# Optimization experiments

Measured on AMD Instinct MI355X. Metric: run time of the kernel, lower is better.

The kernel has to match this reference:

```python
import jax, jax.numpy as jnp
import numpy as np

B, C, D, E, ES, TOPK = 8, 4096, 1024, 16, 256, 4096

def setup_inputs() -> dict:
    key = jax.random.key(0)
    k1, k2, k3, k4 = jax.random.split(key, 4)
    x = jax.random.normal(k1, (B, C, D), dtype=jnp.float32)
    gate = jax.random.normal(k2, (C, E), dtype=jnp.float32) / np.sqrt(D)
    lin1_weight = jax.random.normal(k3, (D, E, ES), dtype=jnp.float32) / np.sqrt(D)
    lin2_weight = jax.random.normal(k4, (E, ES, D), dtype=jnp.float32) / np.sqrt(ES)
    return {"x": x, "gate": gate, "lin1_weight": lin1_weight, "lin2_weight": lin2_weight, "topk": TOPK}

def reference(x, gate, lin1_weight, lin2_weight, topk):
    b, c, d = x.shape
    e = gate.shape[1]
    n_tokens = b * c
    # faithful to original einsum: sum x over dmodel, elementwise-mult by gate[c, e]
    gate_out = jnp.einsum('bcd,ce->bce', x, gate)            # [b, c, e]
    gate_out = jnp.transpose(gate_out, (2, 0, 1)).reshape(e, n_tokens)
    gate_out = jax.nn.softmax(gate_out, axis=1)              # softmax over tokens per expert
    topk_values, topk_indices = jax.lax.top_k(gate_out, topk)  # [e, k]
    xf = x.reshape(n_tokens, d)
    flat_idx = topk_indices.reshape(-1)
    gathered = xf[flat_idx].reshape(e, topk, d)              # dispatch
    h = jax.nn.relu(jnp.einsum('ekd,des->eks', gathered, lin1_weight))
    out = jnp.einsum('eks,esd->ekd', h, lin2_weight)
    out = out * topk_values[..., None]                       # weight by gate probs
    z = jnp.zeros_like(xf).at[flat_idx].add(out.reshape(-1, d))  # scatter-add combine
    return z.reshape(b, c, d)
```

## Files before the change

### kernel.cpp

```cpp
#include <hip/hip_runtime.h>
#include <hip/hip_bf16.h>

#define BB 8
#define CC 4096
#define DD 1024
#define EE 16
#define ESS 256
#define KSEL 4096
#define NTOK (BB*CC)

typedef short bf16x8 __attribute__((ext_vector_type(8)));
typedef float f32x4 __attribute__((ext_vector_type(4)));
typedef unsigned u32x4 __attribute__((ext_vector_type(4)));

struct PickRes { unsigned tau; unsigned n_gt; unsigned n_tie; float sm; };

__device__ __forceinline__ short f2bf(float f) {
  unsigned u = __float_as_uint(f);
  u += 0x7FFFu + ((u >> 16) & 1u);
  return (short)(u >> 16);
}
__device__ __forceinline__ float bf2f(short s) {
  return __uint_as_float(((unsigned)(unsigned short)s) << 16);
}
__device__ __forceinline__ unsigned f2key(float f) {
  unsigned u = __float_as_uint(f);
  return (u & 0x80000000u) ? ~u : (u | 0x80000000u);
}

#define ASG __attribute__((address_space(1)))
#define ASL __attribute__((address_space(3)))
__device__ __forceinline__ void gl_lds16(void* l, const void* g) {
  __builtin_amdgcn_global_load_lds((ASG const unsigned*)g, (ASL unsigned*)l, 16, 0, 0);
}

__global__ void k_logits(const float* __restrict__ x, const float* __restrict__ gate,
                         float* __restrict__ logits, short* __restrict__ xb,
                         int* __restrict__ inv) {
  int wid = threadIdx.x >> 6, lane = threadIdx.x & 63;
  int t = blockIdx.x * 4 + wid;
  const float4* xr = reinterpret_cast<const float4*>(x + (size_t)t * DD);
  short4* xw = reinterpret_cast<short4*>(xb + (size_t)t * DD);
  float s = 0.f;
#pragma unroll
  for (int i = 0; i < 4; ++i) {
    float4 v = xr[lane + 64 * i];
    s += v.x + v.y + v.z + v.w;
    short4 p;
    p.x = f2bf(v.x); p.y = f2bf(v.y); p.z = f2bf(v.z); p.w = f2bf(v.w);
    xw[lane + 64 * i] = p;
  }
#pragma unroll
  for (int off = 32; off; off >>= 1) s += __shfl_xor(s, off);
  if (lane < EE) {
    int c = t & (CC - 1);
    logits[(size_t)lane * NTOK + t] = s * gate[c * EE + lane];
    inv[(size_t)t * EE + lane] = -1;
  }
}

__global__ __launch_bounds__(1024) void k_hist(const float* __restrict__ logits,
                                               unsigned* __restrict__ ghist,
                                               float* __restrict__ separt) {
  int e = blockIdx.x & 15, seg = blockIdx.x >> 4;
  const float* L = logits + (size_t)e * NTOK + seg * 4096;
  unsigned* Hh = ghist + (size_t)e * 65536;
  int tid = threadIdx.x;
  float sl = 0.f;
#pragma unroll
  for (int i = 0; i < 4; ++i) {
    float lv = L[tid + 1024 * i];
    atomicAdd(&Hh[f2key(lv) >> 16], 1u);
    sl += expf(lv);
  }
  __shared__ float red[1024];
  red[tid] = sl; __syncthreads();
  for (int s2 = 512; s2; s2 >>= 1) {
    if (tid < s2) red[tid] += red[tid + s2];
    __syncthreads();
  }
  if (tid == 0) separt[e * 8 + seg] = red[0];
}

__global__ __launch_bounds__(1024) void k_pick(const unsigned* __restrict__ ghist,
                                               const float* __restrict__ logits,
                                               const float* __restrict__ separt,
                                               PickRes* __restrict__ pres) {
  int e = blockIdx.x;
  const unsigned* Hh = ghist + (size_t)e * 65536;
  const float* L = logits + (size_t)e * NTOK;
  int tid = threadIdx.x;
  __shared__ unsigned u0[1024], u1[1024];
  __shared__ unsigned hist256[256];
  __shared__ unsigned sh_b16, sh_ngt, sh_kth;
  __shared__ unsigned sh_p24, sh_ngt2, sh_kth2;

  unsigned cs = 0;
  for (int j = 0; j < 64; ++j) cs += Hh[tid * 64 + j];
  u0[tid] = cs; __syncthreads();
  unsigned* src = u0; unsigned* dst = u1;
  for (int d2 = 1; d2 < 1024; d2 <<= 1) {
    unsigned v = src[tid] + ((tid + d2 < 1024) ? src[tid + d2] : 0u);
    dst[tid] = v; __syncthreads();
    unsigned* tmp = src; src = dst; dst = tmp;
  }
  unsigned kth0 = KSEL;
  unsigned above = (tid < 1023) ? src[tid + 1] : 0u;
  if (above < kth0 && kth0 <= src[tid]) {
    unsigned cum = above;
    for (int j = 63; j >= 0; --j) {
      unsigned h = Hh[tid * 64 + j];
      if (cum + h >= kth0) { sh_b16 = (unsigned)(tid * 64 + j); sh_ngt = cum; sh_kth = kth0 - cum; break; }
      cum += h;
    }
  }
  __syncthreads();
  unsigned p16 = sh_b16, ngt1 = sh_ngt, kth1 = sh_kth;

  if (tid < 256) hist256[tid] = 0;
  __syncthreads();
  for (int t = tid; t < NTOK; t += 1024) {
    unsigned key = f2key(L[t]);
    if ((key >> 16) == p16) atomicAdd(&hist256[(key >> 8) & 255], 1u);
  }
  __syncthreads();
  if (tid == 0) {
    unsigned cum = 0; int d = 255;
    for (; d >= 0; --d) { unsigned h = hist256[d]; if (cum + h >= kth1) break; cum += h; }
    sh_p24 = (p16 << 8) | (unsigned)d;
    sh_ngt2 = ngt1 + cum;
    sh_kth2 = kth1 - cum;
  }
  __syncthreads();
  unsigned p24 = sh_p24, ngt2 = sh_ngt2, kth2 = sh_kth2;

  if (tid < 256) hist256[tid] = 0;
  __syncthreads();
  for (int t = tid; t < NTOK; t += 1024) {
    unsigned key = f2key(L[t]);
    if ((key >> 8) == p24) atomicAdd(&hist256[key & 255], 1u);
  }
  __syncthreads();
  if (tid == 0) {
    unsigned cum = 0; int d = 255;
    for (; d >= 0; --d) { unsigned h = hist256[d]; if (cum + h >= kth2) break; cum += h; }
    unsigned tau = (p24 << 8) | (unsigned)d;
    unsigned n_gt = ngt2 + cum;
    float sm = 0.f;
    for (int j = 0; j < 8; ++j) sm += separt[e * 8 + j];
    PickRes pr; pr.tau = tau; pr.n_gt = n_gt; pr.n_tie = KSEL - n_gt; pr.sm = sm;
    pres[e] = pr;
  }
}

__global__ __launch_bounds__(1024) void k_count(const float* __restrict__ logits,
                                                const PickRes* __restrict__ pres,
                                                unsigned* __restrict__ cnts) {
  int e = blockIdx.x & 15, seg = blockIdx.x >> 4;
  PickRes pr = pres[e];
  const float* L = logits + (size_t)e * NTOK + seg * 4096;
  int tid = threadIdx.x;
  unsigned pk = 0;
#pragma unroll
  for (int i = 0; i < 4; ++i) {
    unsigned key = f2key(L[tid + 1024 * i]);
    pk += (key > pr.tau) ? 0x10000u : ((key == pr.tau) ? 1u : 0u);
  }
  __shared__ unsigned red[1024];
  red[tid] = pk; __syncthreads();
  for (int s2 = 512; s2; s2 >>= 1) {
    if (tid < s2) red[tid] += red[tid + s2];
    __syncthreads();
  }
  if (tid == 0) cnts[e * 8 + seg] = red[0];
}

__global__ void k_scan(const unsigned* __restrict__ cnts, unsigned* __restrict__ bases) {
  int e = threadIdx.x;
  if (e < EE) {
    unsigned gb = 0, qb = 0;
    for (int s = 0; s < 8; ++s) {
      unsigned c = cnts[e * 8 + s];
      bases[e * 8 + s] = (gb << 16) | qb;
      gb += c >> 16; qb += c & 0xFFFFu;
    }
  }
}

__global__ __launch_bounds__(1024) void k_compact(const float* __restrict__ logits,
                                                  const PickRes* __restrict__ pres,
                                                  const unsigned* __restrict__ bases,
                                                  int* __restrict__ sel_idx,
                                                  float* __restrict__ sel_val,
                                                  int* __restrict__ inv) {
  int e = blockIdx.x & 15, seg = blockIdx.x >> 4;
  PickRes pr = pres[e];
  const float* L = logits + (size_t)e * NTOK;
  unsigned b = bases[e * 8 + seg];
  __shared__ unsigned wtg[16], wtq[16];
  __shared__ unsigned base_g, base_q;
  int tid = threadIdx.x, wid = tid >> 6, lane = tid & 63;
  if (tid == 0) { base_g = b >> 16; base_q = b & 0xFFFFu; }
  __syncthreads();
#pragma unroll 1
  for (int i = 0; i < 4; ++i) {
    int t = seg * 4096 + tid + 1024 * i;
    float lv = L[t];
    unsigned key = f2key(lv);
    bool g = key > pr.tau, q = key == pr.tau;
    unsigned long long bg = __ballot(g), bq = __ballot(q);
    unsigned long long lm = (1ull << lane) - 1ull;
    unsigned pg = __popcll(bg & lm), pq = __popcll(bq & lm);
    if (lane == 63) { wtg[wid] = pg + (g ? 1u : 0u); wtq[wid] = pq + (q ? 1u : 0u); }
    __syncthreads();
    unsigned og = base_g, oq = base_q;
    for (int w2 = 0; w2 < wid; ++w2) { og += wtg[w2]; oq += wtq[w2]; }
    unsigned slot = 0xFFFFFFFFu;
    if (g) slot = og + pg;
    else if (q) {
      unsigned r = oq + pq;
      if (r < pr.n_tie) slot = pr.n_gt + r;
    }
    if (slot != 0xFFFFFFFFu) {
      sel_idx[(size_t)e * KSEL + slot] = t;
      sel_val[(size_t)e * KSEL + slot] = expf(lv) / pr.sm;
      inv[(size_t)t * EE + e] = e * KSEL + (int)slot;
    }
    __syncthreads();
    if (tid == 0) {
      unsigned sg = 0, sq = 0;
#pragma unroll
      for (int w2 = 0; w2 < 16; ++w2) { sg += wtg[w2]; sq += wtq[w2]; }
      base_g += sg; base_q += sq;
    }
    __syncthreads();
  }
}

__global__ void k_transpose(const float* __restrict__ src, short* __restrict__ dst,
                            int R, int C) {
  __shared__ float tile[64][65];
  int c0 = blockIdx.x * 64, r0 = blockIdx.y * 64, b = blockIdx.z;
  const float* S = src + (size_t)b * R * C;
  short* Dp = dst + (size_t)b * R * C;
  int tx = threadIdx.x & 63, ty = threadIdx.x >> 6;
#pragma unroll
  for (int i = 0; i < 16; ++i) {
    int r = ty + 4 * i;
    tile[r][tx] = S[(size_t)(r0 + r) * C + c0 + tx];
  }
  __syncthreads();
#pragma unroll
  for (int i = 0; i < 16; ++i) {
    int cR = ty + 4 * i;
    Dp[(size_t)(c0 + cR) * R + r0 + tx] = f2bf(tile[tx][cR]);
  }
}

__global__ __launch_bounds__(512, 4) void k_gemm1(
    const short* __restrict__ xb, const short* __restrict__ W1T,
    const int* __restrict__ sel_idx, const float* __restrict__ sel_val,
    short* __restrict__ H) {
  int bid = blockIdx.x;
  int m0 = ((bid >> 3) & 31) * 128;
  int e = (bid & 7) + ((bid >> 8) << 3);
  __shared__ bf16x8 As8[128 * 8];
  __shared__ bf16x8 Bs8[256 * 8];
  int tid = threadIdx.x, lane = tid & 63, wid = tid >> 6;
  int wr = wid >> 2, wc = wid & 3;
  const int* idxE = sel_idx + (size_t)e * KSEL;
  f32x4 acc[4][4] = {};

  int rowA = tid >> 3, sA = tid & 7;
  int xk = rowA & 7;
  const short* aSrc0 = xb + (size_t)idxE[m0 + rowA] * DD + (sA ^ xk) * 8;
  const short* aSrc1 = xb + (size_t)idxE[m0 + rowA + 64] * DD + (sA ^ xk) * 8;
  const short* wBase = W1T + (size_t)e * ESS * DD + (size_t)rowA * DD + (sA ^ xk) * 8;

  for (int kt = 0; kt < DD / 64; ++kt) {
    int kofs = kt * 64;
    gl_lds16(&As8[tid], aSrc0 + kofs);
    gl_lds16(&As8[512 + tid], aSrc1 + kofs);
#pragma unroll
    for (int j = 0; j < 4; ++j)
      gl_lds16(&Bs8[j * 512 + tid], wBase + (size_t)(64 * j) * DD + kofs);
    __syncthreads();
    bf16x8 af[4][2];
#pragma unroll
    for (int mg = 0; mg < 4; ++mg) {
      int row = wr * 64 + mg * 16 + (lane & 15);
#pragma unroll
      for (int h = 0; h < 2; ++h) {
        int seg = h * 4 + (lane >> 4);
        af[mg][h] = As8[row * 8 + (seg ^ (row & 7))];
      }
    }
#pragma unroll
    for (int ng = 0; ng < 4; ++ng) {
      int rowb = wc * 64 + ng * 16 + (lane & 15);
      bf16x8 b0 = Bs8[rowb * 8 + (((lane >> 4) + 0) ^ (rowb & 7))];
      bf16x8 b1 = Bs8[rowb * 8 + (((lane >> 4) + 4) ^ (rowb & 7))];
#pragma unroll
      for (int mg = 0; mg < 4; ++mg) {
        acc[mg][ng] = __builtin_amdgcn_mfma_f32_16x16x32_bf16(af[mg][0], b0, acc[mg][ng], 0, 0, 0);
        acc[mg][ng] = __builtin_amdgcn_mfma_f32_16x16x32_bf16(af[mg][1], b1, acc[mg][ng], 0, 0, 0);
      }
    }
    __syncthreads();
  }
#pragma unroll
  for (int mg = 0; mg < 4; ++mg) {
#pragma unroll
    for (int r = 0; r < 4; ++r) {
      int ml = wr * 64 + mg * 16 + (lane >> 4) * 4 + r;
      float v = sel_val[(size_t)e * KSEL + m0 + ml];
      short* hrow = H + ((size_t)(e * KSEL + m0 + ml)) * ESS + wc * 64 + (lane & 15);
#pragma unroll
      for (int ng = 0; ng < 4; ++ng) {
        float o = fmaxf(acc[mg][ng][r], 0.f) * v;
        hrow[ng * 16] = f2bf(o);
      }
    }
  }
}

template <int COMBINE>
__global__ __launch_bounds__(512, 4) void k_gemm2(
    const short* __restrict__ H, const short* __restrict__ W2T,
    const int* __restrict__ sel_idx, float* __restrict__ z, short* __restrict__ out) {
  int bid = blockIdx.x;
  int p = (bid & 7) + ((bid >> 8) << 3);
  int m0 = ((bid >> 3) & 31) * 128;
  int n0 = (p & 3) * 256;
  int e = p >> 2;
  __shared__ bf16x8 As8[128 * 8];
  __shared__ bf16x8 Bs8[256 * 8];
  int tid = threadIdx.x, lane = tid & 63, wid = tid >> 6;
  int wr = wid >> 2, wc = wid & 3;
  f32x4 acc[4][4] = {};

  int rowA = tid >> 3, sA = tid & 7;
  int xk = rowA & 7;
  const short* hBase = H + (size_t)(e * KSEL + m0 + rowA) * ESS + (sA ^ xk) * 8;
  const short* w2Base = W2T + (size_t)(e * DD + n0 + rowA) * ESS + (sA ^ xk) * 8;

  for (int kt = 0; kt < ESS / 64; ++kt) {
    int kofs = kt * 64;
    gl_lds16(&As8[tid], hBase + kofs);
    gl_lds16(&As8[512 + tid], hBase + (size_t)64 * ESS + kofs);
#pragma unroll
    for (int j = 0; j < 4; ++j)
      gl_lds16(&Bs8[j * 512 + tid], w2Base + (size_t)(64 * j) * ESS + kofs);
    __syncthreads();
    bf16x8 af[4][2];
#pragma unroll
    for (int mg = 0; mg < 4; ++mg) {
      int row = wr * 64 + mg * 16 + (lane & 15);
#pragma unroll
      for (int h = 0; h < 2; ++h) {
        int seg = h * 4 + (lane >> 4);
        af[mg][h] = As8[row * 8 + (seg ^ (row & 7))];
      }
    }
#pragma unroll
    for (int ng = 0; ng < 4; ++ng) {
      int rowb = wc * 64 + ng * 16 + (lane & 15);
      bf16x8 b0 = Bs8[rowb * 8 + (((lane >> 4) + 0) ^ (rowb & 7))];
      bf16x8 b1 = Bs8[rowb * 8 + (((lane >> 4) + 4) ^ (rowb & 7))];
#pragma unroll
      for (int mg = 0; mg < 4; ++mg) {
        acc[mg][ng] = __builtin_amdgcn_mfma_f32_16x16x32_bf16(af[mg][0], b0, acc[mg][ng], 0, 0, 0);
        acc[mg][ng] = __builtin_amdgcn_mfma_f32_16x16x32_bf16(af[mg][1], b1, acc[mg][ng], 0, 0, 0);
      }
    }
    __syncthreads();
  }
#pragma unroll
  for (int mg = 0; mg < 4; ++mg) {
#pragma unroll
    for (int r = 0; r < 4; ++r) {
      int ml = wr * 64 + mg * 16 + (lane >> 4) * 4 + r;
      if (COMBINE) {
        short* orow = out + ((size_t)(e * KSEL + m0 + ml)) * DD + n0 + wc * 64 + (lane & 15);
#pragma unroll
        for (int ng = 0; ng < 4; ++ng) orow[ng * 16] = f2bf(acc[mg][ng][r]);
      } else {
        int token = sel_idx[(size_t)e * KSEL + m0 + ml];
        float* zr = z + (size_t)token * DD + n0 + wc * 64 + (lane & 15);
#pragma unroll
        for (int ng = 0; ng < 4; ++ng) atomicAdd(zr + ng * 16, acc[mg][ng][r]);
      }
    }
  }
}

__global__ __launch_bounds__(256) void k_combine(const short* __restrict__ out,
                                                 const int* __restrict__ inv,
                                                 float* __restrict__ z) {
  int wid = threadIdx.x >> 6, lane = threadIdx.x & 63;
  int tA = (blockIdx.x * 4 + wid) * 2;
  int tB = tA + 1;
  int gA[16], gB[16];
  const int4* ivA = reinterpret_cast<const int4*>(inv + (size_t)tA * EE);
  const int4* ivB = reinterpret_cast<const int4*>(inv + (size_t)tB * EE);
#pragma unroll
  for (int q = 0; q < 4; ++q) {
    int4 va = ivA[q];
    gA[4 * q] = va.x; gA[4 * q + 1] = va.y; gA[4 * q + 2] = va.z; gA[4 * q + 3] = va.w;
    int4 vb = ivB[q];
    gB[4 * q] = vb.x; gB[4 * q + 1] = vb.y; gB[4 * q + 2] = vb.z; gB[4 * q + 3] = vb.w;
  }
  float accA[16] = {}, accB[16] = {};
#pragma unroll
  for (int e = 0; e < EE; ++e) {
    if (gA[e] >= 0) {
      const u32x4* rp = reinterpret_cast<const u32x4*>(out + (size_t)gA[e] * DD + lane * 16);
      u32x4 v0 = rp[0], v1 = rp[1];
      const short* s0 = reinterpret_cast<const short*>(&v0);
      const short* s1 = reinterpret_cast<const short*>(&v1);
#pragma unroll
      for (int i = 0; i < 8; ++i) accA[i] += bf2f(s0[i]);
#pragma unroll
      for (int i = 0; i < 8; ++i) accA[8 + i] += bf2f(s1[i]);
    }
    if (gB[e] >= 0) {
      const u32x4* rp = reinterpret_cast<const u32x4*>(out + (size_t)gB[e] * DD + lane * 16);
      u32x4 v0 = rp[0], v1 = rp[1];
      const short* s0 = reinterpret_cast<const short*>(&v0);
      const short* s1 = reinterpret_cast<const short*>(&v1);
#pragma unroll
      for (int i = 0; i < 8; ++i) accB[i] += bf2f(s0[i]);
#pragma unroll
      for (int i = 0; i < 8; ++i) accB[8 + i] += bf2f(s1[i]);
    }
  }
  float4* zwA = reinterpret_cast<float4*>(z + (size_t)tA * DD + lane * 16);
  float4* zwB = reinterpret_cast<float4*>(z + (size_t)tB * DD + lane * 16);
#pragma unroll
  for (int i = 0; i < 4; ++i) {
    float4 oa;
    oa.x = accA[4 * i]; oa.y = accA[4 * i + 1]; oa.z = accA[4 * i + 2]; oa.w = accA[4 * i + 3];
    zwA[i] = oa;
    float4 ob;
    ob.x = accB[4 * i]; ob.y = accB[4 * i + 1]; ob.z = accB[4 * i + 2]; ob.w = accB[4 * i + 3];
    zwB[i] = ob;
  }
}

extern "C" void kernel_launch(void* const* d_in, const int* in_sizes, int n_in,
                              void* d_out, int out_size, void* d_ws, size_t ws_size,
                              hipStream_t stream) {
  (void)in_sizes; (void)n_in;
  const float* x = (const float*)d_in[0];
  const float* gate = (const float*)d_in[1];
  const float* lin1 = (const float*)d_in[2];
  const float* lin2 = (const float*)d_in[3];
  float* z = (float*)d_out;

  char* ws = (char*)d_ws;
  size_t off = 0;
  auto alloc = [&](size_t bytes) -> void* {
    off = (off + 255) & ~(size_t)255;
    void* p = ws + off;
    off += bytes;
    return p;
  };
  float* logits = (float*)alloc((size_t)EE * NTOK * 4);
  int* sidx = (int*)alloc((size_t)EE * KSEL * 4);
  float* sval = (float*)alloc((size_t)EE * KSEL * 4);
  int* inv = (int*)alloc((size_t)NTOK * EE * 4);
  short* W1T = (short*)alloc((size_t)EE * ESS * DD * 2);
  short* W2T = (short*)alloc((size_t)EE * DD * ESS * 2);
  short* H = (short*)alloc((size_t)EE * KSEL * ESS * 2);
  short* xb = (short*)alloc((size_t)NTOK * DD * 2);
  size_t out_bytes = (size_t)EE * KSEL * DD * 2;
  bool combine = (off + 256 + out_bytes) <= ws_size;
  short* outbuf = combine ? (short*)alloc(out_bytes) : nullptr;

  unsigned* ghist = (unsigned*)H;
  float* separt = (float*)((char*)H + (size_t)EE * 65536 * 4);
  PickRes* pres = (PickRes*)((char*)separt + 1024);
  unsigned* cnts = (unsigned*)((char*)pres + 1024);
  unsigned* bases = (unsigned*)((char*)cnts + 1024);

  k_transpose<<<dim3(64, 16, 1), 256, 0, stream>>>(lin1, W1T, DD, EE * ESS);
  k_transpose<<<dim3(16, 4, 16), 256, 0, stream>>>(lin2, W2T, ESS, DD);
  k_logits<<<NTOK / 4, 256, 0, stream>>>(x, gate, logits, xb, inv);
  hipMemsetAsync(ghist, 0, (size_t)EE * 65536 * 4, stream);
  k_hist<<<128, 1024, 0, stream>>>(logits, ghist, separt);
  k_pick<<<EE, 1024, 0, stream>>>(ghist, logits, separt, pres);
  k_count<<<128, 1024, 0, stream>>>(logits, pres, cnts);
  k_scan<<<1, 64, 0, stream>>>(cnts, bases);
  k_compact<<<128, 1024, 0, stream>>>(logits, pres, bases, sidx, sval, inv);
  k_gemm1<<<512, 512, 0, stream>>>(xb, W1T, sidx, sval, H);
  if (combine) {
    k_gemm2<1><<<2048, 512, 0, stream>>>(H, W2T, sidx, z, outbuf);
    k_combine<<<NTOK / 8, 256, 0, stream>>>(outbuf, inv, z);
  } else {
    hipMemsetAsync(d_out, 0, (size_t)out_size * sizeof(float), stream);
    k_gemm2<0><<<2048, 512, 0, stream>>>(H, W2T, sidx, z, nullptr);
  }
}
```

Before: 328.0 us.

## Fold count and scan into pick kernel; stage GEMM epilogues through LDS

Removes the separate k_count and k_scan launches. k_pick now counts greater-than and tie keys per segment using wave ballots and shared-memory atomics, then writes the per-segment bases itself. Both GEMM epilogues (gemm1's H output and gemm2's combine output) now stage bf16 results in swizzled LDS and write 16-byte vectors to global memory instead of scattered 2-byte stores. The cost is that a 16-block kernel rescans all logits serially per expert, which may take longer than the 128-block count it replaces, plus extra LDS syncs in the epilogues.

Result: slower. 1.012 ms (+208.4%).

```diff
diff --git a/kernel.cpp b/kernel.cpp
--- a/kernel.cpp
+++ b/kernel.cpp
@@ -85,7 +85,8 @@
 __global__ __launch_bounds__(1024) void k_pick(const unsigned* __restrict__ ghist,
                                                const float* __restrict__ logits,
                                                const float* __restrict__ separt,
-                                               PickRes* __restrict__ pres) {
+                                               PickRes* __restrict__ pres,
+                                               unsigned* __restrict__ bases) {
   int e = blockIdx.x;
   const unsigned* Hh = ghist + (size_t)e * 65536;
   const float* L = logits + (size_t)e * NTOK;
@@ -94,6 +95,8 @@
   __shared__ unsigned hist256[256];
   __shared__ unsigned sh_b16, sh_ngt, sh_kth;
   __shared__ unsigned sh_p24, sh_ngt2, sh_kth2;
+  __shared__ unsigned sh_tau;
+  __shared__ unsigned sgc[8], sqc[8];
 
   unsigned cs = 0;
   for (int j = 0; j < 64; ++j) cs += Hh[tid * 64 + j];
@@ -150,39 +153,27 @@
     for (int j = 0; j < 8; ++j) sm += separt[e * 8 + j];
     PickRes pr; pr.tau = tau; pr.n_gt = n_gt; pr.n_tie = KSEL - n_gt; pr.sm = sm;
     pres[e] = pr;
-  }
-}
-
-__global__ __launch_bounds__(1024) void k_count(const float* __restrict__ logits,
-                                                const PickRes* __restrict__ pres,
-                                                unsigned* __restrict__ cnts) {
-  int e = blockIdx.x & 15, seg = blockIdx.x >> 4;
-  PickRes pr = pres[e];
-  const float* L = logits + (size_t)e * NTOK + seg * 4096;
-  int tid = threadIdx.x;
-  unsigned pk = 0;
-#pragma unroll
-  for (int i = 0; i < 4; ++i) {
-    unsigned key = f2key(L[tid + 1024 * i]);
-    pk += (key > pr.tau) ? 0x10000u : ((key == pr.tau) ? 1u : 0u);
-  }
-  __shared__ unsigned red[1024];
-  red[tid] = pk; __syncthreads();
-  for (int s2 = 512; s2; s2 >>= 1) {
-    if (tid < s2) red[tid] += red[tid + s2];
-    __syncthreads();
-  }
-  if (tid == 0) cnts[e * 8 + seg] = red[0];
-}
-
-__global__ void k_scan(const unsigned* __restrict__ cnts, unsigned* __restrict__ bases) {
-  int e = threadIdx.x;
-  if (e < EE) {
+    sh_tau = tau;
+  }
+  if (tid < 8) { sgc[tid] = 0; sqc[tid] = 0; }
+  __syncthreads();
+  unsigned tau = sh_tau;
+  for (int t = tid; t < NTOK; t += 1024) {
+    unsigned key = f2key(L[t]);
+    unsigned long long bg = __ballot(key > tau);
+    unsigned long long bq = __ballot(key == tau);
+    if ((tid & 63) == 0) {
+      int seg = t >> 12;
+      if (bg) atomicAdd(&sgc[seg], (unsigned)__popcll(bg));
+      if (bq) atomicAdd(&sqc[seg], (unsigned)__popcll(bq));
+    }
+  }
+  __syncthreads();
+  if (tid == 0) {
     unsigned gb = 0, qb = 0;
     for (int s = 0; s < 8; ++s) {
-      unsigned c = cnts[e * 8 + s];
       bases[e * 8 + s] = (gb << 16) | qb;
-      gb += c >> 16; qb += c & 0xFFFFu;
+      gb += sgc[s]; qb += sqc[s];
     }
   }
 }
@@ -308,18 +299,35 @@
     }
     __syncthreads();
   }
-#pragma unroll
-  for (int mg = 0; mg < 4; ++mg) {
-#pragma unroll
-    for (int r = 0; r < 4; ++r) {
-      int ml = wr * 64 + mg * 16 + (lane >> 4) * 4 + r;
-      float v = sel_val[(size_t)e * KSEL + m0 + ml];
-      short* hrow = H + ((size_t)(e * KSEL + m0 + ml)) * ESS + wc * 64 + (lane & 15);
-#pragma unroll
-      for (int ng = 0; ng < 4; ++ng) {
-        float o = fmaxf(acc[mg][ng][r], 0.f) * v;
-        hrow[ng * 16] = f2bf(o);
-      }
+  short* rep = reinterpret_cast<short*>(Bs8) + wid * 2048;
+#pragma unroll 1
+  for (int half = 0; half < 2; ++half) {
+    __syncthreads();
+#pragma unroll
+    for (int mh = 0; mh < 2; ++mh) {
+      int mg = half * 2 + mh;
+#pragma unroll
+      for (int r = 0; r < 4; ++r) {
+        int row32 = mh * 16 + (lane >> 4) * 4 + r;
+        int ml = wr * 64 + half * 32 + row32;
+        float v = sel_val[(size_t)e * KSEL + m0 + ml];
+#pragma unroll
+        for (int ng = 0; ng < 4; ++ng) {
+          int col = ng * 16 + (lane & 15);
+          int seg = col >> 3;
+          rep[row32 * 64 + ((seg ^ (row32 & 7)) * 8) + (col & 7)] =
+              f2bf(fmaxf(acc[mg][ng][r], 0.f) * v);
+        }
+      }
+    }
+    __syncthreads();
+#pragma unroll
+    for (int i = 0; i < 4; ++i) {
+      int row32 = (lane >> 3) + i * 8;
+      int seg = lane & 7;
+      bf16x8 vv = *reinterpret_cast<bf16x8*>(&rep[row32 * 64 + ((seg ^ (row32 & 7)) * 8)]);
+      int grow = m0 + wr * 64 + half * 32 + row32;
+      *reinterpret_cast<bf16x8*>(H + (size_t)(e * KSEL + grow) * ESS + wc * 64 + seg * 8) = vv;
     }
   }
 }
@@ -375,16 +383,41 @@
     }
     __syncthreads();
   }
-#pragma unroll
-  for (int mg = 0; mg < 4; ++mg) {
-#pragma unroll
-    for (int r = 0; r < 4; ++r) {
-      int ml = wr * 64 + mg * 16 + (lane >> 4) * 4 + r;
-      if (COMBINE) {
-        short* orow = out + ((size_t)(e * KSEL + m0 + ml)) * DD + n0 + wc * 64 + (lane & 15);
-#pragma unroll
-        for (int ng = 0; ng < 4; ++ng) orow[ng * 16] = f2bf(acc[mg][ng][r]);
-      } else {
+  if (COMBINE) {
+    short* rep = reinterpret_cast<short*>(Bs8) + wid * 2048;
+#pragma unroll 1
+    for (int half = 0; half < 2; ++half) {
+      __syncthreads();
+#pragma unroll
+      for (int mh = 0; mh < 2; ++mh) {
+        int mg = half * 2 + mh;
+#pragma unroll
+        for (int r = 0; r < 4; ++r) {
+          int row32 = mh * 16 + (lane >> 4) * 4 + r;
+#pragma unroll
+          for (int ng = 0; ng < 4; ++ng) {
+            int col = ng * 16 + (lane & 15);
+            int seg = col >> 3;
+            rep[row32 * 64 + ((seg ^ (row32 & 7)) * 8) + (col & 7)] = f2bf(acc[mg][ng][r]);
+          }
+        }
+      }
+      __syncthreads();
+#pragma unroll
+      for (int i = 0; i < 4; ++i) {
+        int row32 = (lane >> 3) + i * 8;
+        int seg = lane & 7;
+        bf16x8 vv = *reinterpret_cast<bf16x8*>(&rep[row32 * 64 + ((seg ^ (row32 & 7)) * 8)]);
+        int grow = m0 + wr * 64 + half * 32 + row32;
+        *reinterpret_cast<bf16x8*>(out + (size_t)(e * KSEL + grow) * DD + n0 + wc * 64 + seg * 8) = vv;
+      }
+    }
+  } else {
+#pragma unroll
+    for (int mg = 0; mg < 4; ++mg) {
+#pragma unroll
+      for (int r = 0; r < 4; ++r) {
+        int ml = wr * 64 + mg * 16 + (lane >> 4) * 4 + r;
         int token = sel_idx[(size_t)e * KSEL + m0 + ml];
         float* zr = z + (size_t)token * DD + n0 + wc * 64 + (lane & 15);
 #pragma unroll
@@ -480,17 +513,14 @@
   unsigned* ghist = (unsigned*)H;
   float* separt = (float*)((char*)H + (size_t)EE * 65536 * 4);
   PickRes* pres = (PickRes*)((char*)separt + 1024);
-  unsigned* cnts = (unsigned*)((char*)pres + 1024);
-  unsigned* bases = (unsigned*)((char*)cnts + 1024);
+  unsigned* bases = (unsigned*)((char*)pres + 1024);
 
   k_transpose<<<dim3(64, 16, 1), 256, 0, stream>>>(lin1, W1T, DD, EE * ESS);
   k_transpose<<<dim3(16, 4, 16), 256, 0, stream>>>(lin2, W2T, ESS, DD);
   k_logits<<<NTOK / 4, 256, 0, stream>>>(x, gate, logits, xb, inv);
   hipMemsetAsync(ghist, 0, (size_t)EE * 65536 * 4, stream);
   k_hist<<<128, 1024, 0, stream>>>(logits, ghist, separt);
-  k_pick<<<EE, 1024, 0, stream>>>(ghist, logits, separt, pres);
-  k_count<<<128, 1024, 0, stream>>>(logits, pres, cnts);
-  k_scan<<<1, 64, 0, stream>>>(cnts, bases);
+  k_pick<<<EE, 1024, 0, stream>>>(ghist, logits, separt, pres, bases);
   k_compact<<<128, 1024, 0, stream>>>(logits, pres, bases, sidx, sval, inv);
   k_gemm1<<<512, 512, 0, stream>>>(xb, W1T, sidx, sval, H);
   if (combine) {
```
